# Performance work log

Measured on AMD Instinct MI355X. Metric: run time of the kernel, lower is better.

## Reference

```python
import jax, jax.numpy as jnp
import numpy as np


def _binarize_act(z):
    # STE: forward = sign(z), backward = d/dz clamp(z,-1,1)
    clipped = jnp.clip(z, -1.0, 1.0)
    return jax.lax.stop_gradient(jnp.sign(z) - clipped) + clipped


def _binarize_weight(w):
    # per-output-channel scaling factor = mean |w| over (in, kh, kw), detached
    scale = jax.lax.stop_gradient(jnp.mean(jnp.abs(w), axis=(1, 2, 3), keepdims=True))
    clipped = jnp.clip(w, -1.0, 1.0)
    return jax.lax.stop_gradient(scale * jnp.sign(w) - clipped) + clipped


def setup_inputs() -> dict:
    key = jax.random.key(0)
    k = jax.random.split(key, 6)
    B, C, H, W = 16, 64, 256, 256
    return {
        "x": jax.random.normal(k[0], (B, C, H, W), dtype=jnp.float32),
        "move0_bias": jax.random.normal(k[1], (1, C, 1, 1), dtype=jnp.float32) * 0.1,
        "conv_weight": jax.random.normal(k[2], (C, C, 3, 3), dtype=jnp.float32) * 0.1,
        "prelu_weight": jnp.full((C,), 0.25, dtype=jnp.float32)
        + jax.random.normal(k[3], (C,), dtype=jnp.float32) * 0.01,
        "pr_bias0": jax.random.normal(k[4], (1, C, 1, 1), dtype=jnp.float32) * 0.1,
        "pr_bias1": jax.random.normal(k[5], (1, C, 1, 1), dtype=jnp.float32) * 0.1,
    }


def reference(x, move0_bias, conv_weight, prelu_weight, pr_bias0, pr_bias1):
    identity = x  # stride=1, out_channels == in_channels -> no downsample / concat
    z = _binarize_act(x + move0_bias)
    bw = _binarize_weight(conv_weight)
    y = jax.lax.conv_general_dilated(
        z, bw, window_strides=(1, 1), padding=((1, 1), (1, 1)),
        dimension_numbers=("NCHW", "OIHW", "NCHW"))
    # RPReLU: bias0 -> per-channel PReLU -> bias1
    y = y + pr_bias0
    a = prelu_weight.reshape(1, -1, 1, 1)
    y = jnp.where(y > 0, y, a * y)
    y = y + pr_bias1
    return y + identity
```

## Files before the change

kernel.cpp:

```cpp
#include <hip/hip_runtime.h>
#include <stdint.h>

#define Bn 16
#define C 64
#define H 256
#define W 256
#define HW (H * W)
#define NHW (Bn * HW)

__global__ void prep_weights(const float* __restrict__ w,
                             uint64_t* __restrict__ wbits,
                             float* __restrict__ scale) {
    int o = blockIdx.x;
    int c = threadIdx.x;
    const float* wp = w + ((size_t)o * C + c) * 9;
    float asum = 0.f;
#pragma unroll
    for (int tap = 0; tap < 9; ++tap) {
        float v = wp[tap];
        asum += fabsf(v);
        uint64_t m = __ballot(v > 0.f);
        if (c == 0) wbits[o * 9 + tap] = m;
    }
#pragma unroll
    for (int off = 32; off > 0; off >>= 1)
        asum += __shfl_down(asum, off);
    if (c == 0) scale[o] = asum * (1.f / 576.f);
}

__global__ __launch_bounds__(256) void pack_z(const float* __restrict__ x,
                                              const float* __restrict__ bias,
                                              uint64_t* __restrict__ zbits) {
    int p = blockIdx.x * 256 + threadIdx.x;
    int n = p >> 16;
    int hw = p & (HW - 1);
    const float* xp = x + (size_t)n * C * HW + hw;
    uint64_t bits = 0;
#pragma unroll
    for (int c = 0; c < C; ++c) {
        float v = xp[(size_t)c * HW] + bias[c];
        bits |= (uint64_t)(v > 0.f) << c;
    }
    zbits[p] = bits;
}

__global__ __launch_bounds__(256) void bconv(const uint64_t* __restrict__ zbits,
                                             const uint64_t* __restrict__ wbits,
                                             const float* __restrict__ scale,
                                             const float* __restrict__ x,
                                             const float* __restrict__ pb0,
                                             const float* __restrict__ aw,
                                             const float* __restrict__ pb1,
                                             float* __restrict__ out) {
    __shared__ uint64_t swb[576];
    __shared__ float sscale[C], spb0[C], sa[C], spb1[C];
    int t = threadIdx.x;
    if (t < C) {
        sscale[t] = scale[t];
        spb0[t]   = pb0[t];
        sa[t]     = aw[t];
        spb1[t]   = pb1[t];
    }
    for (int i = t; i < 576; i += 256) swb[i] = wbits[i];
    __syncthreads();

    int p = blockIdx.x * 256 + t;
    int n = p >> 16;
    int hw = p & (HW - 1);
    int h = hw >> 8;
    int w = hw & (W - 1);

    const uint64_t* zrow = zbits + (size_t)n * HW;
    uint64_t zb[9];
    int vmask[9];
    int nvalid = 0;
#pragma unroll
    for (int dh = -1; dh <= 1; ++dh) {
#pragma unroll
        for (int dw = -1; dw <= 1; ++dw) {
            int tap = (dh + 1) * 3 + (dw + 1);
            int hh = h + dh, ww = w + dw;
            bool valid = ((unsigned)hh < (unsigned)H) && ((unsigned)ww < (unsigned)W);
            vmask[tap] = valid ? -1 : 0;
            nvalid += valid ? 1 : 0;
            zb[tap] = valid ? zrow[hh * W + ww] : 0ull;
        }
    }

    const float* xid = x + (size_t)n * C * HW + hw;
    float* op = out + (size_t)n * C * HW + hw;
    int base = 64 * nvalid;

#pragma unroll 4
    for (int o = 0; o < C; ++o) {
        const uint64_t* wp = &swb[o * 9];
        int s = 0;
#pragma unroll
        for (int tap = 0; tap < 9; ++tap)
            s += vmask[tap] & (int)__popcll(wp[tap] ^ zb[tap]);
        float y = sscale[o] * (float)(base - 2 * s) + spb0[o];
        y = y > 0.f ? y : sa[o] * y;
        y += spb1[o];
        op[(size_t)o * HW] = y + xid[(size_t)o * HW];
    }
}

extern "C" void kernel_launch(void* const* d_in, const int* in_sizes, int n_in,
                              void* d_out, int out_size, void* d_ws, size_t ws_size,
                              hipStream_t stream) {
    const float* x           = (const float*)d_in[0];
    const float* move0_bias  = (const float*)d_in[1];
    const float* conv_weight = (const float*)d_in[2];
    const float* prelu_w     = (const float*)d_in[3];
    const float* pr_bias0    = (const float*)d_in[4];
    const float* pr_bias1    = (const float*)d_in[5];
    float* out = (float*)d_out;

    uint8_t* ws = (uint8_t*)d_ws;
    uint64_t* zbits = (uint64_t*)ws;
    uint64_t* wbits = (uint64_t*)(ws + (size_t)NHW * 8);
    float* scale    = (float*)(ws + (size_t)NHW * 8 + 576 * 8);

    prep_weights<<<64, 64, 0, stream>>>(conv_weight, wbits, scale);
    pack_z<<<NHW / 256, 256, 0, stream>>>(x, move0_bias, zbits);
    bconv<<<NHW / 256, 256, 0, stream>>>(zbits, wbits, scale, x,
                                         pr_bias0, prelu_w, pr_bias1, out);
}
```

Before: 548.3 us.

## Compute four adjacent pixels per thread with shared z-window and edge-column correction

Each thread in pack_z and bconv now handles four consecutive pixels. Loads and stores use float4 vectors, output stores are nontemporal, and the thread loads a 3x6 window of packed z words that the four outputs share. Interior rows skip per-tap validity masking. Left and right image edges are fixed up with precomputed per-output-channel popcount corrections for the edge weight columns, while the top and bottom rows take a fully masked path. This removes redundant neighbour loads and mask arithmetic, at the cost of more registers and a quarter as many threads.

```diff
diff --git a/kernel.cpp b/kernel.cpp
--- a/kernel.cpp
+++ b/kernel.cpp
@@ -7,20 +7,31 @@
 #define W 256
 #define HW (H * W)
 #define NHW (Bn * HW)
+#define PPT 4
+
+typedef float f32x4 __attribute__((ext_vector_type(4)));
 
 __global__ void prep_weights(const float* __restrict__ w,
                              uint64_t* __restrict__ wbits,
-                             float* __restrict__ scale) {
+                             float* __restrict__ scale,
+                             int* __restrict__ edgeL,
+                             int* __restrict__ edgeR) {
     int o = blockIdx.x;
     int c = threadIdx.x;
     const float* wp = w + ((size_t)o * C + c) * 9;
     float asum = 0.f;
+    uint64_t m[9];
 #pragma unroll
     for (int tap = 0; tap < 9; ++tap) {
         float v = wp[tap];
         asum += fabsf(v);
-        uint64_t m = __ballot(v > 0.f);
-        if (c == 0) wbits[o * 9 + tap] = m;
+        m[tap] = __ballot(v > 0.f);
+    }
+    if (c == 0) {
+#pragma unroll
+        for (int tap = 0; tap < 9; ++tap) wbits[o * 9 + tap] = m[tap];
+        edgeL[o] = 2 * (int)(__popcll(m[0]) + __popcll(m[3]) + __popcll(m[6]));
+        edgeR[o] = 2 * (int)(__popcll(m[2]) + __popcll(m[5]) + __popcll(m[8]));
     }
 #pragma unroll
     for (int off = 32; off > 0; off >>= 1)
@@ -31,22 +42,31 @@
 __global__ __launch_bounds__(256) void pack_z(const float* __restrict__ x,
                                               const float* __restrict__ bias,
                                               uint64_t* __restrict__ zbits) {
-    int p = blockIdx.x * 256 + threadIdx.x;
-    int n = p >> 16;
-    int hw = p & (HW - 1);
+    int t = blockIdx.x * 256 + threadIdx.x;
+    int p0 = t * PPT;
+    int n = p0 >> 16;
+    int hw = p0 & (HW - 1);
     const float* xp = x + (size_t)n * C * HW + hw;
-    uint64_t bits = 0;
-#pragma unroll
+    uint64_t b0 = 0, b1 = 0, b2 = 0, b3 = 0;
+#pragma unroll 8
     for (int c = 0; c < C; ++c) {
-        float v = xp[(size_t)c * HW] + bias[c];
-        bits |= (uint64_t)(v > 0.f) << c;
-    }
-    zbits[p] = bits;
+        f32x4 v = *reinterpret_cast<const f32x4*>(xp + (size_t)c * HW);
+        float bc = bias[c];
+        b0 |= (uint64_t)(v.x + bc > 0.f) << c;
+        b1 |= (uint64_t)(v.y + bc > 0.f) << c;
+        b2 |= (uint64_t)(v.z + bc > 0.f) << c;
+        b3 |= (uint64_t)(v.w + bc > 0.f) << c;
+    }
+    ulonglong2* zp = reinterpret_cast<ulonglong2*>(zbits + p0);
+    zp[0] = make_ulonglong2(b0, b1);
+    zp[1] = make_ulonglong2(b2, b3);
 }
 
 __global__ __launch_bounds__(256) void bconv(const uint64_t* __restrict__ zbits,
                                              const uint64_t* __restrict__ wbits,
                                              const float* __restrict__ scale,
+                                             const int* __restrict__ edgeL,
+                                             const int* __restrict__ edgeR,
                                              const float* __restrict__ x,
                                              const float* __restrict__ pb0,
                                              const float* __restrict__ aw,
@@ -54,54 +74,114 @@
                                              float* __restrict__ out) {
     __shared__ uint64_t swb[576];
     __shared__ float sscale[C], spb0[C], sa[C], spb1[C];
+    __shared__ int sEL[C], sER[C];
     int t = threadIdx.x;
     if (t < C) {
         sscale[t] = scale[t];
         spb0[t]   = pb0[t];
         sa[t]     = aw[t];
         spb1[t]   = pb1[t];
+        sEL[t]    = edgeL[t];
+        sER[t]    = edgeR[t];
     }
     for (int i = t; i < 576; i += 256) swb[i] = wbits[i];
     __syncthreads();
 
-    int p = blockIdx.x * 256 + t;
-    int n = p >> 16;
-    int hw = p & (HW - 1);
-    int h = hw >> 8;
-    int w = hw & (W - 1);
-
-    const uint64_t* zrow = zbits + (size_t)n * HW;
-    uint64_t zb[9];
-    int vmask[9];
-    int nvalid = 0;
-#pragma unroll
-    for (int dh = -1; dh <= 1; ++dh) {
-#pragma unroll
-        for (int dw = -1; dw <= 1; ++dw) {
-            int tap = (dh + 1) * 3 + (dw + 1);
-            int hh = h + dh, ww = w + dw;
-            bool valid = ((unsigned)hh < (unsigned)H) && ((unsigned)ww < (unsigned)W);
-            vmask[tap] = valid ? -1 : 0;
-            nvalid += valid ? 1 : 0;
-            zb[tap] = valid ? zrow[hh * W + ww] : 0ull;
+    int p0 = (blockIdx.x * 256 + t) * PPT;
+    int n  = p0 >> 16;
+    int hw = p0 & (HW - 1);
+    int h  = hw >> 8;
+    int w0 = hw & (W - 1);
+
+    const uint64_t* zr = zbits + (size_t)n * HW;
+    uint64_t zb[3][6];
+#pragma unroll
+    for (int i = 0; i < 3; ++i) {
+        int hh = h - 1 + i;
+        bool rv = (unsigned)hh < (unsigned)H;
+#pragma unroll
+        for (int j = 0; j < 6; ++j) {
+            int cc = w0 - 1 + j;
+            bool cv = (unsigned)cc < (unsigned)W;
+            zb[i][j] = (rv && cv) ? zr[hh * W + cc] : 0ull;
         }
     }
 
     const float* xid = x + (size_t)n * C * HW + hw;
     float* op = out + (size_t)n * C * HW + hw;
-    int base = 64 * nvalid;
-
-#pragma unroll 4
-    for (int o = 0; o < C; ++o) {
-        const uint64_t* wp = &swb[o * 9];
-        int s = 0;
-#pragma unroll
-        for (int tap = 0; tap < 9; ++tap)
-            s += vmask[tap] & (int)__popcll(wp[tap] ^ zb[tap]);
-        float y = sscale[o] * (float)(base - 2 * s) + spb0[o];
-        y = y > 0.f ? y : sa[o] * y;
-        y += spb1[o];
-        op[(size_t)o * HW] = y + xid[(size_t)o * HW];
+
+    bool leftE  = (w0 == 0);
+    bool rightE = (w0 == W - PPT);
+
+    if (h >= 1 && h <= H - 2) {
+#pragma unroll 2
+        for (int o = 0; o < C; ++o) {
+            const uint64_t* wp = &swb[o * 9];
+            int s0 = 0, s1 = 0, s2 = 0, s3 = 0;
+#pragma unroll
+            for (int i = 0; i < 3; ++i)
+#pragma unroll
+                for (int jj = 0; jj < 3; ++jj) {
+                    uint64_t wt = wp[i * 3 + jj];
+                    s0 += (int)__popcll(wt ^ zb[i][jj]);
+                    s1 += (int)__popcll(wt ^ zb[i][jj + 1]);
+                    s2 += (int)__popcll(wt ^ zb[i][jj + 2]);
+                    s3 += (int)__popcll(wt ^ zb[i][jj + 3]);
+                }
+            int d0 = 576 - 2 * s0, d1 = 576 - 2 * s1;
+            int d2 = 576 - 2 * s2, d3 = 576 - 2 * s3;
+            if (leftE)  d0 += sEL[o] - 192;
+            if (rightE) d3 += sER[o] - 192;
+
+            float sc = sscale[o], bb0 = spb0[o], af = sa[o], bb1 = spb1[o];
+            f32x4 idv = *reinterpret_cast<const f32x4*>(xid + (size_t)o * HW);
+            f32x4 r;
+            float y;
+            y = sc * (float)d0 + bb0; y = y > 0.f ? y : af * y; r.x = y + bb1 + idv.x;
+            y = sc * (float)d1 + bb0; y = y > 0.f ? y : af * y; r.y = y + bb1 + idv.y;
+            y = sc * (float)d2 + bb0; y = y > 0.f ? y : af * y; r.z = y + bb1 + idv.z;
+            y = sc * (float)d3 + bb0; y = y > 0.f ? y : af * y; r.w = y + bb1 + idv.w;
+            __builtin_nontemporal_store(r, reinterpret_cast<f32x4*>(op + (size_t)o * HW));
+        }
+    } else {
+        int vrow[3], vcol[6];
+#pragma unroll
+        for (int i = 0; i < 3; ++i)
+            vrow[i] = ((unsigned)(h - 1 + i) < (unsigned)H) ? -1 : 0;
+#pragma unroll
+        for (int j = 0; j < 6; ++j)
+            vcol[j] = ((unsigned)(w0 - 1 + j) < (unsigned)W) ? -1 : 0;
+        int nv[4];
+#pragma unroll
+        for (int q = 0; q < 4; ++q) {
+            int nr = (vrow[0] & 1) + (vrow[1] & 1) + (vrow[2] & 1);
+            int nc = (vcol[q] & 1) + (vcol[q + 1] & 1) + (vcol[q + 2] & 1);
+            nv[q] = nr * nc;
+        }
+#pragma unroll 2
+        for (int o = 0; o < C; ++o) {
+            const uint64_t* wp = &swb[o * 9];
+            int s[4] = {0, 0, 0, 0};
+#pragma unroll
+            for (int i = 0; i < 3; ++i)
+#pragma unroll
+                for (int jj = 0; jj < 3; ++jj) {
+                    uint64_t wt = wp[i * 3 + jj];
+#pragma unroll
+                    for (int q = 0; q < 4; ++q)
+                        s[q] += (vrow[i] & vcol[q + jj]) &
+                                (int)__popcll(wt ^ zb[i][q + jj]);
+                }
+            float sc = sscale[o], bb0 = spb0[o], af = sa[o], bb1 = spb1[o];
+            f32x4 idv = *reinterpret_cast<const f32x4*>(xid + (size_t)o * HW);
+            f32x4 r;
+            float y;
+            y = sc * (float)(64 * nv[0] - 2 * s[0]) + bb0; y = y > 0.f ? y : af * y; r.x = y + bb1 + idv.x;
+            y = sc * (float)(64 * nv[1] - 2 * s[1]) + bb0; y = y > 0.f ? y : af * y; r.y = y + bb1 + idv.y;
+            y = sc * (float)(64 * nv[2] - 2 * s[2]) + bb0; y = y > 0.f ? y : af * y; r.z = y + bb1 + idv.z;
+            y = sc * (float)(64 * nv[3] - 2 * s[3]) + bb0; y = y > 0.f ? y : af * y; r.w = y + bb1 + idv.w;
+            __builtin_nontemporal_store(r, reinterpret_cast<f32x4*>(op + (size_t)o * HW));
+        }
     }
 }
 
@@ -120,9 +200,11 @@
     uint64_t* zbits = (uint64_t*)ws;
     uint64_t* wbits = (uint64_t*)(ws + (size_t)NHW * 8);
     float* scale    = (float*)(ws + (size_t)NHW * 8 + 576 * 8);
-
-    prep_weights<<<64, 64, 0, stream>>>(conv_weight, wbits, scale);
-    pack_z<<<NHW / 256, 256, 0, stream>>>(x, move0_bias, zbits);
-    bconv<<<NHW / 256, 256, 0, stream>>>(zbits, wbits, scale, x,
-                                         pr_bias0, prelu_w, pr_bias1, out);
-}
+    int* edgeL      = (int*)(ws + (size_t)NHW * 8 + 576 * 8 + 256);
+    int* edgeR      = (int*)(ws + (size_t)NHW * 8 + 576 * 8 + 512);
+
+    prep_weights<<<64, 64, 0, stream>>>(conv_weight, wbits, scale, edgeL, edgeR);
+    pack_z<<<NHW / PPT / 256, 256, 0, stream>>>(x, move0_bias, zbits);
+    bconv<<<NHW / PPT / 256, 256, 0, stream>>>(zbits, wbits, scale, edgeL, edgeR,
+                                               x, pr_bias0, prelu_w, pr_bias1, out);
+}
```

Result: no change. 540.2 us (-1.5%).
